# Kernel tuning notes

Hardware: AMD Instinct MI355X
Metric: run time of the kernel (lower is better)

## Reference

```python
import jax, jax.numpy as jnp
import numpy as np

N = 100000      # nodes
E = 1600000     # edges
F_IN = 64       # num_node_features
HID = 128       # hidden_channels
HEADS = 8       # heads in gat1
G = 1000        # number of graphs
EPS = 1e-5


def _layer_norm(x, gamma, beta):
    mu = jnp.mean(x, axis=-1, keepdims=True)
    var = jnp.var(x, axis=-1, keepdims=True)
    return (x - mu) * jax.lax.rsqrt(var + EPS) * gamma + beta


def _gat_conv(x, src, dst, W, a_src, a_dst, b):
    # PyG GATConv (concat=True, negative_slope=0.2, self-loops already in src/dst)
    n = x.shape[0]
    heads, c = a_src.shape
    h = (x @ W).reshape(n, heads, c)                      # [N,H,C]
    alpha_s = jnp.sum(h * a_src[None], axis=-1)           # [N,H]
    alpha_d = jnp.sum(h * a_dst[None], axis=-1)           # [N,H]
    e = jax.nn.leaky_relu(alpha_s[src] + alpha_d[dst], 0.2)   # [Etot,H]
    m = jax.ops.segment_max(e, dst, num_segments=n)       # per-dst max (stable softmax)
    e = jnp.exp(e - m[dst])
    denom = jax.ops.segment_sum(e, dst, num_segments=n)
    attn = e / (denom[dst] + 1e-16)                        # [Etot,H]
    out = jax.ops.segment_sum(h[src] * attn[:, :, None], dst, num_segments=n)
    return out.reshape(n, heads * c) + b


def setup_inputs():
    key = jax.random.key(0)
    ks = jax.random.split(key, 32)
    s = 0.05
    inp = {
        'x': jax.random.normal(ks[0], (N, F_IN), dtype=jnp.float32),
        'edge_index': jax.random.randint(ks[1], (2, E), 0, N),
        'batch': jnp.sort(jax.random.randint(ks[2], (N,), 0, G)),
        # gat1: 64 -> 16 per head, 8 heads
        'W1': jax.random.normal(ks[3], (F_IN, HID), dtype=jnp.float32) * s,
        'as1': jax.random.normal(ks[4], (HEADS, HID // HEADS), dtype=jnp.float32) * s,
        'ad1': jax.random.normal(ks[5], (HEADS, HID // HEADS), dtype=jnp.float32) * s,
        'b1': jnp.zeros((HID,), dtype=jnp.float32),
        # gat2: 128 -> 128, 1 head
        'W2': jax.random.normal(ks[6], (HID, HID), dtype=jnp.float32) * s,
        'as2': jax.random.normal(ks[7], (1, HID), dtype=jnp.float32) * s,
        'ad2': jax.random.normal(ks[8], (1, HID), dtype=jnp.float32) * s,
        'b2': jnp.zeros((HID,), dtype=jnp.float32),
        # gat3
        'W3': jax.random.normal(ks[9], (HID, HID), dtype=jnp.float32) * s,
        'as3': jax.random.normal(ks[10], (1, HID), dtype=jnp.float32) * s,
        'ad3': jax.random.normal(ks[11], (1, HID), dtype=jnp.float32) * s,
        'b3': jnp.zeros((HID,), dtype=jnp.float32),
        # layer norms
        'g1': jnp.ones((HID,), dtype=jnp.float32), 'be1': jnp.zeros((HID,), dtype=jnp.float32),
        'g2': jnp.ones((HID,), dtype=jnp.float32), 'be2': jnp.zeros((HID,), dtype=jnp.float32),
        'g3': jnp.ones((HID,), dtype=jnp.float32), 'be3': jnp.zeros((HID,), dtype=jnp.float32),
        # linear heads
        'lw1': jax.random.normal(ks[12], (HID, HID), dtype=jnp.float32) * s,
        'lb1': jnp.zeros((HID,), dtype=jnp.float32),
        'lw2': jax.random.normal(ks[13], (HID, HID), dtype=jnp.float32) * s,
        'lb2': jnp.zeros((HID,), dtype=jnp.float32),
    }
    return inp


def reference(x, edge_index, batch, W1, as1, ad1, b1, W2, as2, ad2, b2,
              W3, as3, ad3, b3, g1, be1, g2, be2, g3, be3, lw1, lb1, lw2, lb2):
    n = x.shape[0]
    loops = jnp.arange(n)
    src = jnp.concatenate([edge_index[0], loops])   # add self-loops (PyG default)
    dst = jnp.concatenate([edge_index[1], loops])

    h = _gat_conv(x, src, dst, W1, as1, ad1, b1)
    h = _layer_norm(jax.nn.elu(h), g1, be1)          # dropout is identity in eval

    idn2 = h
    h = _gat_conv(h, src, dst, W2, as2, ad2, b2)
    h = _layer_norm(jax.nn.elu(h), g2, be2) + idn2

    idn3 = h
    h = _gat_conv(h, src, dst, W3, as3, ad3, b3)
    h = _layer_norm(jax.nn.elu(h), g3, be3) + idn3

    # global mean pool over graphs
    sums = jax.ops.segment_sum(h, batch, num_segments=G)
    cnt = jax.ops.segment_sum(jnp.ones((n, 1), h.dtype), batch, num_segments=G)
    pooled = sums / jnp.maximum(cnt, 1.0)

    out = jax.nn.elu(pooled @ lw1 + lb1)
    return out @ lw2 + lb2
```

## Files before the change

kernel.cpp:

```cpp
#include <hip/hip_runtime.h>
#include <hip/hip_bf16.h>
#include <cstdint>
#include <cstddef>

constexpr int F_IN = 64;
constexpr int HID  = 128;
constexpr int SCHUNK = 4096;

typedef __attribute__((ext_vector_type(8))) short short8v;
typedef __attribute__((ext_vector_type(4))) float f32x4;
typedef __attribute__((ext_vector_type(8))) unsigned short ushort8v;

__device__ __forceinline__ float bf2f(unsigned short u) {
  return __uint_as_float((unsigned)u << 16);
}
__device__ __forceinline__ unsigned short f2bf(float x) {
  unsigned u = __float_as_uint(x);
  u += 0x7FFFu + ((u >> 16) & 1u);
  return (unsigned short)(u >> 16);
}

__global__ __launch_bounds__(256) void k_bhist(const int* __restrict__ ei,
                                               int* __restrict__ bcnt, int E) {
  __shared__ int hist[1024];
  int t = threadIdx.x;
  for (int k = t; k < 1024; k += 256) hist[k] = 0;
  __syncthreads();
  for (int i = blockIdx.x * 256 + t; i < E; i += gridDim.x * 256)
    atomicAdd(&hist[ei[E + i] >> 7], 1);
  __syncthreads();
  for (int k = t; k < 1024; k += 256)
    if (hist[k]) atomicAdd(&bcnt[k], hist[k]);
}

__global__ __launch_bounds__(1024) void k_bscan(const int* __restrict__ bcnt,
                                                int* __restrict__ boff,
                                                int* __restrict__ bcur, int nb) {
  __shared__ int tmp[1024];
  int t = threadIdx.x;
  int v = (t < nb) ? bcnt[t] : 0;
  tmp[t] = v;
  __syncthreads();
  #pragma unroll
  for (int off = 1; off < 1024; off <<= 1) {
    int x = tmp[t];
    int add = (t >= off) ? tmp[t - off] : 0;
    __syncthreads();
    tmp[t] = x + add;
    __syncthreads();
  }
  if (t < nb) {
    int ex = tmp[t] - v;
    boff[t] = ex;
    bcur[t] = ex;
    if (t == nb - 1) boff[nb] = tmp[t];
  }
}

__global__ __launch_bounds__(256) void k_bscat(const int* __restrict__ ei,
                                               int* __restrict__ bcur,
                                               uint2* __restrict__ pairs, int E) {
  __shared__ int lh[1024];
  __shared__ int lc[1024];
  int t = threadIdx.x;
  int start = blockIdx.x * SCHUNK;
  if (start >= E) return;
  int end = min(start + SCHUNK, E);
  for (int k = t; k < 1024; k += 256) { lh[k] = 0; lc[k] = 0; }
  __syncthreads();
  int dreg[SCHUNK / 256];
  #pragma unroll
  for (int q = 0; q < SCHUNK / 256; ++q) {
    int i = start + q * 256 + t;
    int d = (i < end) ? ei[E + i] : -1;
    dreg[q] = d;
    if (d >= 0) atomicAdd(&lh[d >> 7], 1);
  }
  __syncthreads();
  for (int k = t; k < 1024; k += 256) {
    int c = lh[k];
    lh[k] = (c > 0) ? atomicAdd(&bcur[k], c) : 0;
  }
  __syncthreads();
  #pragma unroll
  for (int q = 0; q < SCHUNK / 256; ++q) {
    int i = start + q * 256 + t;
    int d = dreg[q];
    if (d < 0) continue;
    int s = ei[i];
    int b = d >> 7;
    int loc = atomicAdd(&lc[b], 1);
    pairs[lh[b] + loc] = make_uint2((unsigned)s, (unsigned)d);
  }
}

__global__ __launch_bounds__(256) void k_bfin(const uint2* __restrict__ pairs,
                                              const int* __restrict__ boff,
                                              int* __restrict__ row_off,
                                              int* __restrict__ csr_src,
                                              int n, int E) {
  __shared__ int ldeg[128];
  __shared__ int lcur[128];
  int b = blockIdx.x;
  int t = threadIdx.x;
  int pb = boff[b], pe = boff[b + 1];
  int fullbase = pb + min(b << 7, n);
  int idx = (b << 7) + t;
  if (t < 128) ldeg[t] = (idx < n) ? 1 : 0;
  __syncthreads();
  for (int j = pb + t; j < pe; j += 256)
    atomicAdd(&ldeg[pairs[j].y & 127], 1);
  __syncthreads();
  int cnt = (t < 128) ? ldeg[t] : 0;
  for (int off = 1; off < 128; off <<= 1) {
    int add = (t < 128 && t >= off) ? ldeg[t - off] : 0;
    __syncthreads();
    if (t < 128) ldeg[t] += add;
    __syncthreads();
  }
  if (t < 128) {
    int base = fullbase + ldeg[t] - cnt;
    if (idx < n) {
      row_off[idx] = base;
      csr_src[base] = idx;
      lcur[t] = base + 1;
    } else lcur[t] = base;
  }
  if (b == 0 && t == 255) row_off[n] = E + n;
  __syncthreads();
  for (int j = pb + t; j < pe; j += 256) {
    uint2 pr = pairs[j];
    int pos = atomicAdd(&lcur[pr.y & 127], 1);
    csr_src[pos] = (int)pr.x;
  }
}

__global__ void k_tobf4(const float4* __restrict__ X, ushort4* __restrict__ Y,
                        int total4) {
  int i = blockIdx.x * 256 + threadIdx.x;
  if (i >= total4) return;
  float4 v = X[i];
  ushort4 o;
  o.x = f2bf(v.x); o.y = f2bf(v.y); o.z = f2bf(v.z); o.w = f2bf(v.w);
  Y[i] = o;
}

__global__ void k_wpack3(const float* __restrict__ W1, const float* __restrict__ W2,
                         const float* __restrict__ W3, unsigned short* __restrict__ Wf1,
                         unsigned short* __restrict__ Wf2, unsigned short* __restrict__ Wf3) {
  int i = blockIdx.x * 256 + threadIdx.x;
  const float* W; unsigned short* Wf; int idx;
  if (i < 8192)       { W = W1; Wf = Wf1; idx = i; }
  else if (i < 24576) { W = W2; Wf = Wf2; idx = i - 8192; }
  else if (i < 40960) { W = W3; Wf = Wf3; idx = i - 24576; }
  else return;
  int j    = idx & 7;
  int lane = (idx >> 3) & 63;
  int t    = (idx >> 9) & 7;
  int ks   = idx >> 12;
  int k = ks * 32 + (lane >> 4) * 8 + j;
  int c = t * 16 + (lane & 15);
  Wf[idx] = f2bf(W[k * 128 + c]);
}

template<int K, int HEADS>
__global__ __launch_bounds__(256) void k_mgemm(const short* __restrict__ Xb,
                                               const short* __restrict__ Wf,
                                               const float* __restrict__ a_s,
                                               const float* __restrict__ a_d,
                                               unsigned short* __restrict__ Y,
                                               float* __restrict__ AS,
                                               float* __restrict__ AD, int n) {
  int wv   = threadIdx.x >> 6;
  int lane = threadIdx.x & 63;
  int r0   = blockIdx.x * 64 + wv * 16;
  int ln = lane & 15, kg = lane >> 4;
  f32x4 acc[8] = {};
  int arow = min(r0 + ln, n - 1);
  const short* aptr = Xb + arow * K + kg * 8;
  #pragma unroll
  for (int ks = 0; ks < K / 32; ++ks) {
    short8v a = *(const short8v*)(aptr + ks * 32);
    const short* wp = Wf + ks * 4096 + lane * 8;
    #pragma unroll
    for (int t = 0; t < 8; ++t) {
      short8v b = *(const short8v*)(wp + t * 512);
      acc[t] = __builtin_amdgcn_mfma_f32_16x16x32_bf16(a, b, acc[t], 0, 0, 0);
    }
  }
  float asv[8], adv[8];
  #pragma unroll
  for (int t = 0; t < 8; ++t) { asv[t] = a_s[t * 16 + ln]; adv[t] = a_d[t * 16 + ln]; }
  #pragma unroll
  for (int reg = 0; reg < 4; ++reg) {
    int r = r0 + kg * 4 + reg;
    bool valid = (r < n);
    if (HEADS == 1) {
      float s1 = 0.f, s2 = 0.f;
      #pragma unroll
      for (int t = 0; t < 8; ++t) {
        s1 = fmaf(acc[t][reg], asv[t], s1);
        s2 = fmaf(acc[t][reg], adv[t], s2);
      }
      #pragma unroll
      for (int off = 1; off < 16; off <<= 1) {
        s1 += __shfl_xor(s1, off);
        s2 += __shfl_xor(s2, off);
      }
      if (valid && ln == 0) { AS[r] = s1; AD[r] = s2; }
    } else {
      float s1[8], s2[8];
      #pragma unroll
      for (int t = 0; t < 8; ++t) {
        s1[t] = acc[t][reg] * asv[t];
        s2[t] = acc[t][reg] * adv[t];
      }
      #pragma unroll
      for (int off = 1; off < 16; off <<= 1) {
        #pragma unroll
        for (int t = 0; t < 8; ++t) {
          s1[t] += __shfl_xor(s1[t], off);
          s2[t] += __shfl_xor(s2[t], off);
        }
      }
      float w1 = s1[0], w2 = s2[0];
      #pragma unroll
      for (int t = 1; t < 8; ++t) {
        w1 = (ln == t) ? s1[t] : w1;
        w2 = (ln == t) ? s2[t] : w2;
      }
      if (valid && ln < 8) { AS[r * 8 + ln] = w1; AD[r * 8 + ln] = w2; }
    }
  }
  #pragma unroll
  for (int t = 0; t < 8; ++t) {
    #pragma unroll
    for (int reg = 0; reg < 4; ++reg) {
      int r = r0 + kg * 4 + reg;
      if (r < n) Y[r * 128 + t * 16 + ln] = f2bf(acc[t][reg]);
    }
  }
}

template<int LOGC>
__global__ __launch_bounds__(256) void k_agg_post(const unsigned short* __restrict__ Hu,
    const int* __restrict__ row_off, const int* __restrict__ csr_src,
    const float* __restrict__ AS, const float* __restrict__ AD,
    const float* __restrict__ bias, const unsigned short* __restrict__ RES,
    const float* __restrict__ gamma, const float* __restrict__ beta,
    unsigned short* __restrict__ Yb, int n, int has_res) {
  if constexpr (LOGC >= 7) {
    int tid = blockIdx.x * 256 + threadIdx.x;
    int wid = tid >> 4;
    int ll  = threadIdx.x & 15;
    if (wid >= n) return;
    int c = ll << 3;
    int sbase = (threadIdx.x & 63) & ~15;
    float adv = AD[wid];
    int jb = row_off[wid], je = row_off[wid + 1];
    float den = 0.f, a[8] = {};
    for (int j0 = jb; j0 < je; j0 += 16) {
      int cnt = min(16, je - j0);
      int s_l = 0; float p_l = 0.f;
      if (ll < cnt) {
        s_l = csr_src[j0 + ll];
        float e = AS[s_l] + adv;
        e = (e > 0.f) ? e : 0.2f * e;
        p_l = __expf(e);
      }
      int k = 0;
      for (; k + 8 <= cnt; k += 8) {
        int sk[8]; float pk[8]; ushort8v uu[8];
        #pragma unroll
        for (int q = 0; q < 8; ++q) sk[q] = __shfl(s_l, sbase | (k + q));
        #pragma unroll
        for (int q = 0; q < 8; ++q) uu[q] = *(const ushort8v*)(Hu + (sk[q] << 7) + c);
        #pragma unroll
        for (int q = 0; q < 8; ++q) pk[q] = __shfl(p_l, sbase | (k + q));
        #pragma unroll
        for (int q = 0; q < 8; ++q) {
          den += pk[q];
          #pragma unroll
          for (int m = 0; m < 8; ++m) a[m] = fmaf(pk[q], bf2f(uu[q][m]), a[m]);
        }
      }
      for (; k < cnt; ++k) {
        int   s  = __shfl(s_l, sbase | k);
        float pk = __shfl(p_l, sbase | k);
        ushort8v u = *(const ushort8v*)(Hu + (s << 7) + c);
        den += pk;
        #pragma unroll
        for (int m = 0; m < 8; ++m) a[m] = fmaf(pk, bf2f(u[m]), a[m]);
      }
    }
    float inv = 1.f / (den + 1e-16f);
    float4 bv0 = *(const float4*)(bias + c);
    float4 bv1 = *(const float4*)(bias + c + 4);
    float e[8];
    float bb[8] = {bv0.x, bv0.y, bv0.z, bv0.w, bv1.x, bv1.y, bv1.z, bv1.w};
    #pragma unroll
    for (int m = 0; m < 8; ++m) {
      float t = a[m] * inv + bb[m];
      e[m] = t > 0.f ? t : __expf(t) - 1.f;
    }
    float s1 = 0.f, s2 = 0.f;
    #pragma unroll
    for (int m = 0; m < 8; ++m) { s1 += e[m]; s2 += e[m] * e[m]; }
    #pragma unroll
    for (int off = 1; off < 16; off <<= 1) {
      s1 += __shfl_xor(s1, off);
      s2 += __shfl_xor(s2, off);
    }
    float mu  = s1 * (1.f / 128.f);
    float var = s2 * (1.f / 128.f) - mu * mu;
    float rs  = rsqrtf(var + 1e-5f);
    int base = wid * HID;
    float rr[8] = {};
    if (has_res) {
      ushort8v rv = *(const ushort8v*)(RES + base + c);
      #pragma unroll
      for (int m = 0; m < 8; ++m) rr[m] = bf2f(rv[m]);
    }
    float4 gv0 = *(const float4*)(gamma + c);
    float4 gv1 = *(const float4*)(gamma + c + 4);
    float4 tv0 = *(const float4*)(beta + c);
    float4 tv1 = *(const float4*)(beta + c + 4);
    float gg[8] = {gv0.x, gv0.y, gv0.z, gv0.w, gv1.x, gv1.y, gv1.z, gv1.w};
    float tt[8] = {tv0.x, tv0.y, tv0.z, tv0.w, tv1.x, tv1.y, tv1.z, tv1.w};
    ushort8v ob;
    #pragma unroll
    for (int m = 0; m < 8; ++m) ob[m] = f2bf((e[m] - mu) * rs * gg[m] + tt[m] + rr[m]);
    *(ushort8v*)(Yb + base + c) = ob;
  } else {
    int tid = blockIdx.x * 256 + threadIdx.x;
    int wid = tid >> 5;
    int ll  = threadIdx.x & 31;
    if (wid >= n) return;
    constexpr int NH  = HID >> LOGC;
    constexpr int SEG = 1 << (LOGC - 2);
    int abslane = threadIdx.x & 63;
    int c = ll << 2;
    int h = c >> LOGC;
    int r = ll & (SEG - 1);
    int sbase = abslane & ~(SEG - 1);
    float adv = AD[wid * NH + h];
    int jb = row_off[wid], je = row_off[wid + 1];
    float den = 0.f, a0 = 0.f, a1 = 0.f, a2 = 0.f, a3 = 0.f;
    for (int j0 = jb; j0 < je; j0 += SEG) {
      int cnt = min(SEG, je - j0);
      int s_l = 0; float p_l = 0.f;
      if (r < cnt) {
        s_l = csr_src[j0 + r];
        float e = AS[s_l * NH + h] + adv;
        e = (e > 0.f) ? e : 0.2f * e;
        p_l = __expf(e);
      }
      int k = 0;
      for (; k + 4 <= cnt; k += 4) {
        int sk0 = __shfl(s_l, sbase | k);
        int sk1 = __shfl(s_l, sbase | (k + 1));
        int sk2 = __shfl(s_l, sbase | (k + 2));
        int sk3 = __shfl(s_l, sbase | (k + 3));
        ushort4 u0 = *(const ushort4*)(Hu + (sk0 << 7) + c);
        ushort4 u1 = *(const ushort4*)(Hu + (sk1 << 7) + c);
        ushort4 u2 = *(const ushort4*)(Hu + (sk2 << 7) + c);
        ushort4 u3 = *(const ushort4*)(Hu + (sk3 << 7) + c);
        float p0 = __shfl(p_l, sbase | k);
        float p1 = __shfl(p_l, sbase | (k + 1));
        float p2 = __shfl(p_l, sbase | (k + 2));
        float p3 = __shfl(p_l, sbase | (k + 3));
        den += (p0 + p1) + (p2 + p3);
        a0 = fmaf(p0, bf2f(u0.x), a0); a1 = fmaf(p0, bf2f(u0.y), a1);
        a2 = fmaf(p0, bf2f(u0.z), a2); a3 = fmaf(p0, bf2f(u0.w), a3);
        a0 = fmaf(p1, bf2f(u1.x), a0); a1 = fmaf(p1, bf2f(u1.y), a1);
        a2 = fmaf(p1, bf2f(u1.z), a2); a3 = fmaf(p1, bf2f(u1.w), a3);
        a0 = fmaf(p2, bf2f(u2.x), a0); a1 = fmaf(p2, bf2f(u2.y), a1);
        a2 = fmaf(p2, bf2f(u2.z), a2); a3 = fmaf(p2, bf2f(u2.w), a3);
        a0 = fmaf(p3, bf2f(u3.x), a0); a1 = fmaf(p3, bf2f(u3.y), a1);
        a2 = fmaf(p3, bf2f(u3.z), a2); a3 = fmaf(p3, bf2f(u3.w), a3);
      }
      for (; k < cnt; ++k) {
        int   s  = __shfl(s_l, sbase | k);
        float pk = __shfl(p_l, sbase | k);
        ushort4 u = *(const ushort4*)(Hu + (s << 7) + c);
        den += pk;
        a0 = fmaf(pk, bf2f(u.x), a0); a1 = fmaf(pk, bf2f(u.y), a1);
        a2 = fmaf(pk, bf2f(u.z), a2); a3 = fmaf(pk, bf2f(u.w), a3);
      }
    }
    float inv = 1.f / (den + 1e-16f);
    float4 bv = *(const float4*)(bias + c);
    float t0 = a0 * inv + bv.x;
    float t1 = a1 * inv + bv.y;
    float t2 = a2 * inv + bv.z;
    float t3 = a3 * inv + bv.w;
    float e0 = t0 > 0.f ? t0 : __expf(t0) - 1.f;
    float e1 = t1 > 0.f ? t1 : __expf(t1) - 1.f;
    float e2 = t2 > 0.f ? t2 : __expf(t2) - 1.f;
    float e3 = t3 > 0.f ? t3 : __expf(t3) - 1.f;
    float s1 = (e0 + e1) + (e2 + e3);
    float s2 = (e0 * e0 + e1 * e1) + (e2 * e2 + e3 * e3);
    #pragma unroll
    for (int off = 16; off >= 1; off >>= 1) {
      s1 += __shfl_xor(s1, off);
      s2 += __shfl_xor(s2, off);
    }
    float mu  = s1 * (1.f / 128.f);
    float var = s2 * (1.f / 128.f) - mu * mu;
    float rs  = rsqrtf(var + 1e-5f);
    int base = wid * HID;
    float r0 = 0.f, r1 = 0.f, r2 = 0.f, r3 = 0.f;
    if (has_res) {
      ushort4 rv = *(const ushort4*)(RES + base + c);
      r0 = bf2f(rv.x); r1 = bf2f(rv.y); r2 = bf2f(rv.z); r3 = bf2f(rv.w);
    }
    float4 gv = *(const float4*)(gamma + c);
    float4 betv = *(const float4*)(beta + c);
    ushort4 ob;
    ob.x = f2bf((e0 - mu) * rs * gv.x + betv.x + r0);
    ob.y = f2bf((e1 - mu) * rs * gv.y + betv.y + r1);
    ob.z = f2bf((e2 - mu) * rs * gv.z + betv.z + r2);
    ob.w = f2bf((e3 - mu) * rs * gv.w + betv.w + r3);
    *(ushort4*)(Yb + base + c) = ob;
  }
}

__global__ __launch_bounds__(128) void k_head(const unsigned short* __restrict__ Hf,
    const int* __restrict__ batch, const float* __restrict__ lw1,
    const float* __restrict__ lb1, const float* __restrict__ lw2,
    const float* __restrict__ lb2, float* __restrict__ out, int n) {
  __shared__ float pooled[128];
  __shared__ float h1[128];
  int g = blockIdx.x;
  int c = threadIdx.x;
  int lo = 0, hi = n;
  while (lo < hi) { int mid = (lo + hi) >> 1; if (batch[mid] < g) lo = mid + 1; else hi = mid; }
  int start = lo;
  hi = n;
  while (lo < hi) { int mid = (lo + hi) >> 1; if (batch[mid] < g + 1) lo = mid + 1; else hi = mid; }
  int end = lo;
  float s = 0.f;
  for (int i = start; i < end; ++i) s += bf2f(Hf[(size_t)i * 128 + c]);
  pooled[c] = s / (float)max(end - start, 1);
  __syncthreads();
  float acc = lb1[c];
  #pragma unroll 8
  for (int k = 0; k < 128; ++k) acc = fmaf(pooled[k], lw1[k * 128 + c], acc);
  h1[c] = acc > 0.f ? acc : __expf(acc) - 1.f;
  __syncthreads();
  float acc2 = lb2[c];
  #pragma unroll 8
  for (int k = 0; k < 128; ++k) acc2 = fmaf(h1[k], lw2[k * 128 + c], acc2);
  out[(size_t)g * 128 + c] = acc2;
}

extern "C" void kernel_launch(void* const* d_in, const int* in_sizes, int n_in,
                              void* d_out, int out_size, void* d_ws, size_t ws_size,
                              hipStream_t stream) {
  const float* x   = (const float*)d_in[0];
  const int*   ei  = (const int*)d_in[1];
  const int*   bat = (const int*)d_in[2];
  const float* W1  = (const float*)d_in[3];
  const float* as1 = (const float*)d_in[4];
  const float* ad1 = (const float*)d_in[5];
  const float* b1  = (const float*)d_in[6];
  const float* W2  = (const float*)d_in[7];
  const float* as2 = (const float*)d_in[8];
  const float* ad2 = (const float*)d_in[9];
  const float* b2  = (const float*)d_in[10];
  const float* W3  = (const float*)d_in[11];
  const float* as3 = (const float*)d_in[12];
  const float* ad3 = (const float*)d_in[13];
  const float* b3  = (const float*)d_in[14];
  const float* g1  = (const float*)d_in[15];
  const float* be1 = (const float*)d_in[16];
  const float* g2  = (const float*)d_in[17];
  const float* be2 = (const float*)d_in[18];
  const float* g3  = (const float*)d_in[19];
  const float* be3 = (const float*)d_in[20];
  const float* lw1 = (const float*)d_in[21];
  const float* lb1 = (const float*)d_in[22];
  const float* lw2 = (const float*)d_in[23];
  const float* lb2 = (const float*)d_in[24];

  int N = in_sizes[0] / F_IN;
  int E = in_sizes[1] / 2;
  int G = out_size / HID;
  int tot = E + N;
  int nb  = (N + 127) >> 7;

  char* p = (char*)d_ws;
  auto alloc = [&](size_t bytes) { char* r = p; p += (bytes + 511) & ~(size_t)511; return r; };
  int*   bcnt    = (int*)  alloc(1024 * 4);
  int*   boff    = (int*)  alloc(1025 * 4);
  int*   bcur    = (int*)  alloc(1024 * 4);
  int*   row_off = (int*)  alloc((size_t)(N + 1) * 4);
  int*   csr_src = (int*)  alloc((size_t)tot * 4);
  uint2* pairs   = (uint2*)alloc((size_t)E * 8);
  float* AS      = (float*)alloc((size_t)N * 8 * 4);
  float* AD      = (float*)alloc((size_t)N * 8 * 4);
  unsigned short* Hb  = (unsigned short*)alloc((size_t)N * HID * 2);
  unsigned short* Fb0 = (unsigned short*)alloc((size_t)N * HID * 2);
  unsigned short* Fb1 = (unsigned short*)alloc((size_t)N * HID * 2);
  unsigned short* Fb2 = (unsigned short*)alloc((size_t)N * HID * 2);
  unsigned short* Wf1 = (unsigned short*)alloc(64 * 128 * 2);
  unsigned short* Wf2 = (unsigned short*)alloc(128 * 128 * 2);
  unsigned short* Wf3 = (unsigned short*)alloc(128 * 128 * 2);
  unsigned short* xb  = (unsigned short*)pairs;

  (void)hipMemsetAsync(bcnt, 0, 1024 * 4, stream);

  int sb = (E + SCHUNK - 1) / SCHUNK;
  k_bhist<<<256, 256, 0, stream>>>(ei, bcnt, E);
  k_bscan<<<1, 1024, 0, stream>>>(bcnt, boff, bcur, nb);
  k_bscat<<<sb, 256, 0, stream>>>(ei, bcur, pairs, E);
  k_bfin <<<nb, 256, 0, stream>>>(pairs, boff, row_off, csr_src, N, E);

  k_tobf4 <<<(N * F_IN / 4 + 255) / 256, 256, 0, stream>>>((const float4*)x,
                                                           (ushort4*)xb, N * F_IN / 4);
  k_wpack3<<<160, 256, 0, stream>>>(W1, W2, W3, Wf1, Wf2, Wf3);

  int mb  = (N + 63) / 64;
  int nh4 = (N + 7) / 8;
  int nh7 = (N + 15) / 16;

  k_mgemm<64, 8><<<mb, 256, 0, stream>>>((const short*)xb, (const short*)Wf1,
                                         as1, ad1, Hb, AS, AD, N);
  k_agg_post<4><<<nh4, 256, 0, stream>>>(Hb, row_off, csr_src, AS, AD, b1,
                                         nullptr, g1, be1, Fb0, N, 0);

  k_mgemm<128, 1><<<mb, 256, 0, stream>>>((const short*)Fb0, (const short*)Wf2,
                                          as2, ad2, Hb, AS, AD, N);
  k_agg_post<7><<<nh7, 256, 0, stream>>>(Hb, row_off, csr_src, AS, AD, b2,
                                         Fb0, g2, be2, Fb1, N, 1);

  k_mgemm<128, 1><<<mb, 256, 0, stream>>>((const short*)Fb1, (const short*)Wf3,
                                          as3, ad3, Hb, AS, AD, N);
  k_agg_post<7><<<nh7, 256, 0, stream>>>(Hb, row_off, csr_src, AS, AD, b3,
                                         Fb1, g3, be3, Fb2, N, 1);

  k_head<<<G, 128, 0, stream>>>(Fb2, bat, lw1, lb1, lw2, lb2, (float*)d_out, N);
}
```

Baseline: 429.5 us.

## Split GAT aggregation into edge-softmax, column-sliced gather, and post LayerNorm kernels

The GEMM output now goes to a column-sliced layout: eight 16-channel slabs of N×16 bf16. A separate edge kernel precomputes normalized attention weights per edge, and per head for layer 1. A sliced aggregation kernel then gathers 32-byte rows from one slab per block, so each slab (about 3.2 MB) can stay cache-resident while the random neighbor gathers run, and a post kernel applies ELU, LayerNorm and the residual. The cost is extra launches, an attention buffer written and read (up to 8×(E+N) floats for layer 1), csr_src read eight times, and a bf16 round-trip of the pre-activation through T.

```diff
diff --git a/kernel.cpp b/kernel.cpp
--- a/kernel.cpp
+++ b/kernel.cpp
@@ -170,7 +170,7 @@
                                                const float* __restrict__ a_d,
                                                unsigned short* __restrict__ Y,
                                                float* __restrict__ AS,
-                                               float* __restrict__ AD, int n) {
+                                               float* __restrict__ AD, int n, int n16) {
   int wv   = threadIdx.x >> 6;
   int lane = threadIdx.x & 63;
   int r0   = blockIdx.x * 64 + wv * 16;
@@ -237,192 +237,147 @@
     #pragma unroll
     for (int reg = 0; reg < 4; ++reg) {
       int r = r0 + kg * 4 + reg;
-      if (r < n) Y[r * 128 + t * 16 + ln] = f2bf(acc[t][reg]);
+      if (r < n) Y[t * n16 + r * 16 + ln] = f2bf(acc[t][reg]);
     }
   }
 }
 
-template<int LOGC>
-__global__ __launch_bounds__(256) void k_agg_post(const unsigned short* __restrict__ Hu,
+__global__ __launch_bounds__(256) void k_edgep1(const int* __restrict__ row_off,
+    const int* __restrict__ csr_src, const float* __restrict__ AS,
+    const float* __restrict__ AD, float* __restrict__ attn, int n) {
+  int tid = blockIdx.x * 256 + threadIdx.x;
+  int wid = tid >> 4;
+  int ll  = threadIdx.x & 15;
+  if (wid >= n) return;
+  float adv = AD[wid];
+  int jb = row_off[wid], je = row_off[wid + 1];
+  float den = 0.f;
+  for (int j = jb + ll; j < je; j += 16) {
+    int s = csr_src[j];
+    float e = AS[s] + adv;
+    e = (e > 0.f) ? e : 0.2f * e;
+    float p = __expf(e);
+    attn[j] = p;
+    den += p;
+  }
+  #pragma unroll
+  for (int off = 1; off < 16; off <<= 1) den += __shfl_xor(den, off);
+  float inv = 1.f / (den + 1e-16f);
+  for (int j = jb + ll; j < je; j += 16) attn[j] *= inv;
+}
+
+__global__ __launch_bounds__(256) void k_edgep8(const int* __restrict__ row_off,
+    const int* __restrict__ csr_src, const float* __restrict__ AS,
+    const float* __restrict__ AD, float* __restrict__ attn, int AE, int n) {
+  int tid = blockIdx.x * 256 + threadIdx.x;
+  int wid = tid >> 5;
+  int ll  = threadIdx.x & 31;
+  if (wid >= n) return;
+  int e = ll >> 3, h = ll & 7;
+  float adv = AD[wid * 8 + h];
+  int jb = row_off[wid], je = row_off[wid + 1];
+  float den = 0.f;
+  for (int j = jb + e; j < je; j += 4) {
+    int s = csr_src[j];
+    float x = AS[s * 8 + h] + adv;
+    x = (x > 0.f) ? x : 0.2f * x;
+    float p = __expf(x);
+    attn[h * AE + j] = p;
+    den += p;
+  }
+  den += __shfl_xor(den, 8);
+  den += __shfl_xor(den, 16);
+  float inv = 1.f / (den + 1e-16f);
+  for (int j = jb + e; j < je; j += 4) attn[h * AE + j] *= inv;
+}
+
+__global__ __launch_bounds__(256) void k_aggs(const unsigned short* __restrict__ Hs,
     const int* __restrict__ row_off, const int* __restrict__ csr_src,
-    const float* __restrict__ AS, const float* __restrict__ AD,
-    const float* __restrict__ bias, const unsigned short* __restrict__ RES,
-    const float* __restrict__ gamma, const float* __restrict__ beta,
-    unsigned short* __restrict__ Yb, int n, int has_res) {
-  if constexpr (LOGC >= 7) {
-    int tid = blockIdx.x * 256 + threadIdx.x;
-    int wid = tid >> 4;
-    int ll  = threadIdx.x & 15;
-    if (wid >= n) return;
-    int c = ll << 3;
-    int sbase = (threadIdx.x & 63) & ~15;
-    float adv = AD[wid];
-    int jb = row_off[wid], je = row_off[wid + 1];
-    float den = 0.f, a[8] = {};
-    for (int j0 = jb; j0 < je; j0 += 16) {
-      int cnt = min(16, je - j0);
-      int s_l = 0; float p_l = 0.f;
-      if (ll < cnt) {
-        s_l = csr_src[j0 + ll];
-        float e = AS[s_l] + adv;
-        e = (e > 0.f) ? e : 0.2f * e;
-        p_l = __expf(e);
-      }
-      int k = 0;
-      for (; k + 8 <= cnt; k += 8) {
-        int sk[8]; float pk[8]; ushort8v uu[8];
-        #pragma unroll
-        for (int q = 0; q < 8; ++q) sk[q] = __shfl(s_l, sbase | (k + q));
-        #pragma unroll
-        for (int q = 0; q < 8; ++q) uu[q] = *(const ushort8v*)(Hu + (sk[q] << 7) + c);
-        #pragma unroll
-        for (int q = 0; q < 8; ++q) pk[q] = __shfl(p_l, sbase | (k + q));
-        #pragma unroll
-        for (int q = 0; q < 8; ++q) {
-          den += pk[q];
-          #pragma unroll
-          for (int m = 0; m < 8; ++m) a[m] = fmaf(pk[q], bf2f(uu[q][m]), a[m]);
-        }
-      }
-      for (; k < cnt; ++k) {
-        int   s  = __shfl(s_l, sbase | k);
-        float pk = __shfl(p_l, sbase | k);
-        ushort8v u = *(const ushort8v*)(Hu + (s << 7) + c);
-        den += pk;
-        #pragma unroll
-        for (int m = 0; m < 8; ++m) a[m] = fmaf(pk, bf2f(u[m]), a[m]);
-      }
+    const float* __restrict__ attn, int astride, const float* __restrict__ bias,
+    unsigned short* __restrict__ T, int n, int n16) {
+  int s   = blockIdx.x & 7;
+  int grp = blockIdx.x >> 3;
+  int lane = threadIdx.x & 63;
+  int wave = threadIdx.x >> 6;
+  int node = grp * 128 + wave * 32 + (lane >> 1);
+  if (node >= n) return;
+  int half = lane & 1;
+  const unsigned short* Hsl = Hs + (size_t)s * n16;
+  const float* at = attn + (size_t)s * astride;
+  int jb = row_off[node], je = row_off[node + 1];
+  float a[8] = {};
+  int j = jb;
+  for (; j + 8 <= je; j += 8) {
+    int sk[8]; float wk[8]; ushort8v uu[8];
+    #pragma unroll
+    for (int q = 0; q < 8; ++q) sk[q] = __builtin_nontemporal_load(csr_src + j + q);
+    #pragma unroll
+    for (int q = 0; q < 8; ++q) uu[q] = *(const ushort8v*)(Hsl + (sk[q] << 4) + half * 8);
+    #pragma unroll
+    for (int q = 0; q < 8; ++q) wk[q] = __builtin_nontemporal_load(at + j + q);
+    #pragma unroll
+    for (int q = 0; q < 8; ++q) {
+      #pragma unroll
+      for (int m = 0; m < 8; ++m) a[m] = fmaf(wk[q], bf2f(uu[q][m]), a[m]);
     }
-    float inv = 1.f / (den + 1e-16f);
-    float4 bv0 = *(const float4*)(bias + c);
-    float4 bv1 = *(const float4*)(bias + c + 4);
-    float e[8];
-    float bb[8] = {bv0.x, bv0.y, bv0.z, bv0.w, bv1.x, bv1.y, bv1.z, bv1.w};
-    #pragma unroll
-    for (int m = 0; m < 8; ++m) {
-      float t = a[m] * inv + bb[m];
-      e[m] = t > 0.f ? t : __expf(t) - 1.f;
-    }
-    float s1 = 0.f, s2 = 0.f;
-    #pragma unroll
-    for (int m = 0; m < 8; ++m) { s1 += e[m]; s2 += e[m] * e[m]; }
-    #pragma unroll
-    for (int off = 1; off < 16; off <<= 1) {
-      s1 += __shfl_xor(s1, off);
-      s2 += __shfl_xor(s2, off);
-    }
-    float mu  = s1 * (1.f / 128.f);
-    float var = s2 * (1.f / 128.f) - mu * mu;
-    float rs  = rsqrtf(var + 1e-5f);
-    int base = wid * HID;
-    float rr[8] = {};
-    if (has_res) {
-      ushort8v rv = *(const ushort8v*)(RES + base + c);
-      #pragma unroll
-      for (int m = 0; m < 8; ++m) rr[m] = bf2f(rv[m]);
-    }
-    float4 gv0 = *(const float4*)(gamma + c);
-    float4 gv1 = *(const float4*)(gamma + c + 4);
-    float4 tv0 = *(const float4*)(beta + c);
-    float4 tv1 = *(const float4*)(beta + c + 4);
-    float gg[8] = {gv0.x, gv0.y, gv0.z, gv0.w, gv1.x, gv1.y, gv1.z, gv1.w};
-    float tt[8] = {tv0.x, tv0.y, tv0.z, tv0.w, tv1.x, tv1.y, tv1.z, tv1.w};
-    ushort8v ob;
-    #pragma unroll
-    for (int m = 0; m < 8; ++m) ob[m] = f2bf((e[m] - mu) * rs * gg[m] + tt[m] + rr[m]);
-    *(ushort8v*)(Yb + base + c) = ob;
-  } else {
-    int tid = blockIdx.x * 256 + threadIdx.x;
-    int wid = tid >> 5;
-    int ll  = threadIdx.x & 31;
-    if (wid >= n) return;
-    constexpr int NH  = HID >> LOGC;
-    constexpr int SEG = 1 << (LOGC - 2);
-    int abslane = threadIdx.x & 63;
-    int c = ll << 2;
-    int h = c >> LOGC;
-    int r = ll & (SEG - 1);
-    int sbase = abslane & ~(SEG - 1);
-    float adv = AD[wid * NH + h];
-    int jb = row_off[wid], je = row_off[wid + 1];
-    float den = 0.f, a0 = 0.f, a1 = 0.f, a2 = 0.f, a3 = 0.f;
-    for (int j0 = jb; j0 < je; j0 += SEG) {
-      int cnt = min(SEG, je - j0);
-      int s_l = 0; float p_l = 0.f;
-      if (r < cnt) {
-        s_l = csr_src[j0 + r];
-        float e = AS[s_l * NH + h] + adv;
-        e = (e > 0.f) ? e : 0.2f * e;
-        p_l = __expf(e);
-      }
-      int k = 0;
-      for (; k + 4 <= cnt; k += 4) {
-        int sk0 = __shfl(s_l, sbase | k);
-        int sk1 = __shfl(s_l, sbase | (k + 1));
-        int sk2 = __shfl(s_l, sbase | (k + 2));
-        int sk3 = __shfl(s_l, sbase | (k + 3));
-        ushort4 u0 = *(const ushort4*)(Hu + (sk0 << 7) + c);
-        ushort4 u1 = *(const ushort4*)(Hu + (sk1 << 7) + c);
-        ushort4 u2 = *(const ushort4*)(Hu + (sk2 << 7) + c);
-        ushort4 u3 = *(const ushort4*)(Hu + (sk3 << 7) + c);
-        float p0 = __shfl(p_l, sbase | k);
-        float p1 = __shfl(p_l, sbase | (k + 1));
-        float p2 = __shfl(p_l, sbase | (k + 2));
-        float p3 = __shfl(p_l, sbase | (k + 3));
-        den += (p0 + p1) + (p2 + p3);
-        a0 = fmaf(p0, bf2f(u0.x), a0); a1 = fmaf(p0, bf2f(u0.y), a1);
-        a2 = fmaf(p0, bf2f(u0.z), a2); a3 = fmaf(p0, bf2f(u0.w), a3);
-        a0 = fmaf(p1, bf2f(u1.x), a0); a1 = fmaf(p1, bf2f(u1.y), a1);
-        a2 = fmaf(p1, bf2f(u1.z), a2); a3 = fmaf(p1, bf2f(u1.w), a3);
-        a0 = fmaf(p2, bf2f(u2.x), a0); a1 = fmaf(p2, bf2f(u2.y), a1);
-        a2 = fmaf(p2, bf2f(u2.z), a2); a3 = fmaf(p2, bf2f(u2.w), a3);
-        a0 = fmaf(p3, bf2f(u3.x), a0); a1 = fmaf(p3, bf2f(u3.y), a1);
-        a2 = fmaf(p3, bf2f(u3.z), a2); a3 = fmaf(p3, bf2f(u3.w), a3);
-      }
-      for (; k < cnt; ++k) {
-        int   s  = __shfl(s_l, sbase | k);
-        float pk = __shfl(p_l, sbase | k);
-        ushort4 u = *(const ushort4*)(Hu + (s << 7) + c);
-        den += pk;
-        a0 = fmaf(pk, bf2f(u.x), a0); a1 = fmaf(pk, bf2f(u.y), a1);
-        a2 = fmaf(pk, bf2f(u.z), a2); a3 = fmaf(pk, bf2f(u.w), a3);
-      }
-    }
-    float inv = 1.f / (den + 1e-16f);
-    float4 bv = *(const float4*)(bias + c);
-    float t0 = a0 * inv + bv.x;
-    float t1 = a1 * inv + bv.y;
-    float t2 = a2 * inv + bv.z;
-    float t3 = a3 * inv + bv.w;
-    float e0 = t0 > 0.f ? t0 : __expf(t0) - 1.f;
-    float e1 = t1 > 0.f ? t1 : __expf(t1) - 1.f;
-    float e2 = t2 > 0.f ? t2 : __expf(t2) - 1.f;
-    float e3 = t3 > 0.f ? t3 : __expf(t3) - 1.f;
-    float s1 = (e0 + e1) + (e2 + e3);
-    float s2 = (e0 * e0 + e1 * e1) + (e2 * e2 + e3 * e3);
-    #pragma unroll
-    for (int off = 16; off >= 1; off >>= 1) {
-      s1 += __shfl_xor(s1, off);
-      s2 += __shfl_xor(s2, off);
-    }
-    float mu  = s1 * (1.f / 128.f);
-    float var = s2 * (1.f / 128.f) - mu * mu;
-    float rs  = rsqrtf(var + 1e-5f);
-    int base = wid * HID;
-    float r0 = 0.f, r1 = 0.f, r2 = 0.f, r3 = 0.f;
-    if (has_res) {
-      ushort4 rv = *(const ushort4*)(RES + base + c);
-      r0 = bf2f(rv.x); r1 = bf2f(rv.y); r2 = bf2f(rv.z); r3 = bf2f(rv.w);
-    }
-    float4 gv = *(const float4*)(gamma + c);
-    float4 betv = *(const float4*)(beta + c);
-    ushort4 ob;
-    ob.x = f2bf((e0 - mu) * rs * gv.x + betv.x + r0);
-    ob.y = f2bf((e1 - mu) * rs * gv.y + betv.y + r1);
-    ob.z = f2bf((e2 - mu) * rs * gv.z + betv.z + r2);
-    ob.w = f2bf((e3 - mu) * rs * gv.w + betv.w + r3);
-    *(ushort4*)(Yb + base + c) = ob;
-  }
+  }
+  for (; j < je; ++j) {
+    int sv = __builtin_nontemporal_load(csr_src + j);
+    float w = __builtin_nontemporal_load(at + j);
+    ushort8v u = *(const ushort8v*)(Hsl + (sv << 4) + half * 8);
+    #pragma unroll
+    for (int m = 0; m < 8; ++m) a[m] = fmaf(w, bf2f(u[m]), a[m]);
+  }
+  int cbase = s * 16 + half * 8;
+  ushort8v ob;
+  #pragma unroll
+  for (int m = 0; m < 8; ++m) ob[m] = f2bf(a[m] + bias[cbase + m]);
+  *(ushort8v*)(T + (size_t)s * n16 + node * 16 + half * 8) = ob;
+}
+
+__global__ __launch_bounds__(256) void k_post(const unsigned short* __restrict__ T,
+    const unsigned short* __restrict__ RES, const float* __restrict__ gamma,
+    const float* __restrict__ beta, unsigned short* __restrict__ F,
+    int n, int n16, int has_res) {
+  int tid = blockIdx.x * 256 + threadIdx.x;
+  int node = tid >> 4;
+  int ll = threadIdx.x & 15;
+  if (node >= n) return;
+  int sl = ll >> 1, half = ll & 1;
+  ushort8v tv = *(const ushort8v*)(T + (size_t)sl * n16 + node * 16 + half * 8);
+  float e[8];
+  float s1 = 0.f, s2 = 0.f;
+  #pragma unroll
+  for (int m = 0; m < 8; ++m) {
+    float t = bf2f(tv[m]);
+    t = t > 0.f ? t : __expf(t) - 1.f;
+    e[m] = t; s1 += t; s2 += t * t;
+  }
+  #pragma unroll
+  for (int off = 1; off < 16; off <<= 1) {
+    s1 += __shfl_xor(s1, off);
+    s2 += __shfl_xor(s2, off);
+  }
+  float mu  = s1 * (1.f / 128.f);
+  float var = s2 * (1.f / 128.f) - mu * mu;
+  float rs  = rsqrtf(var + 1e-5f);
+  int c = ll * 8;
+  float4 gv0 = *(const float4*)(gamma + c);
+  float4 gv1 = *(const float4*)(gamma + c + 4);
+  float4 bv0 = *(const float4*)(beta + c);
+  float4 bv1 = *(const float4*)(beta + c + 4);
+  float gg[8] = {gv0.x, gv0.y, gv0.z, gv0.w, gv1.x, gv1.y, gv1.z, gv1.w};
+  float bb[8] = {bv0.x, bv0.y, bv0.z, bv0.w, bv1.x, bv1.y, bv1.z, bv1.w};
+  float rr[8] = {};
+  if (has_res) {
+    ushort8v rv = *(const ushort8v*)(RES + (size_t)node * 128 + c);
+    #pragma unroll
+    for (int m = 0; m < 8; ++m) rr[m] = bf2f(rv[m]);
+  }
+  ushort8v ob;
+  #pragma unroll
+  for (int m = 0; m < 8; ++m) ob[m] = f2bf((e[m] - mu) * rs * gg[m] + bb[m] + rr[m]);
+  *(ushort8v*)(F + (size_t)node * 128 + c) = ob;
 }
 
 __global__ __launch_bounds__(128) void k_head(const unsigned short* __restrict__ Hf,
@@ -488,6 +443,7 @@
   int G = out_size / HID;
   int tot = E + N;
   int nb  = (N + 127) >> 7;
+  int n16 = N * 16;
 
   char* p = (char*)d_ws;
   auto alloc = [&](size_t bytes) { char* r = p; p += (bytes + 511) & ~(size_t)511; return r; };
@@ -499,7 +455,9 @@
   uint2* pairs   = (uint2*)alloc((size_t)E * 8);
   float* AS      = (float*)alloc((size_t)N * 8 * 4);
   float* AD      = (float*)alloc((size_t)N * 8 * 4);
-  unsigned short* Hb  = (unsigned short*)alloc((size_t)N * HID * 2);
+  float* attn    = (float*)alloc((size_t)tot * 8 * 4);
+  unsigned short* Hs  = (unsigned short*)alloc((size_t)N * HID * 2);
+  unsigned short* T   = (unsigned short*)alloc((size_t)N * HID * 2);
   unsigned short* Fb0 = (unsigned short*)alloc((size_t)N * HID * 2);
   unsigned short* Fb1 = (unsigned short*)alloc((size_t)N * HID * 2);
   unsigned short* Fb2 = (unsigned short*)alloc((size_t)N * HID * 2);
@@ -521,23 +479,27 @@
   k_wpack3<<<160, 256, 0, stream>>>(W1, W2, W3, Wf1, Wf2, Wf3);
 
   int mb  = (N + 63) / 64;
-  int nh4 = (N + 7) / 8;
-  int nh7 = (N + 15) / 16;
+  int ep1 = (N * 16 + 255) / 256;
+  int ep8 = (N * 32 + 255) / 256;
+  int ags = 8 * ((N + 127) / 128);
 
   k_mgemm<64, 8><<<mb, 256, 0, stream>>>((const short*)xb, (const short*)Wf1,
-                                         as1, ad1, Hb, AS, AD, N);
-  k_agg_post<4><<<nh4, 256, 0, stream>>>(Hb, row_off, csr_src, AS, AD, b1,
-                                         nullptr, g1, be1, Fb0, N, 0);
+                                         as1, ad1, Hs, AS, AD, N, n16);
+  k_edgep8<<<ep8, 256, 0, stream>>>(row_off, csr_src, AS, AD, attn, tot, N);
+  k_aggs  <<<ags, 256, 0, stream>>>(Hs, row_off, csr_src, attn, tot, b1, T, N, n16);
+  k_post  <<<ep1, 256, 0, stream>>>(T, nullptr, g1, be1, Fb0, N, n16, 0);
 
   k_mgemm<128, 1><<<mb, 256, 0, stream>>>((const short*)Fb0, (const short*)Wf2,
-                                          as2, ad2, Hb, AS, AD, N);
-  k_agg_post<7><<<nh7, 256, 0, stream>>>(Hb, row_off, csr_src, AS, AD, b2,
-                                         Fb0, g2, be2, Fb1, N, 1);
+                                          as2, ad2, Hs, AS, AD, N, n16);
+  k_edgep1<<<ep1, 256, 0, stream>>>(row_off, csr_src, AS, AD, attn, N);
+  k_aggs  <<<ags, 256, 0, stream>>>(Hs, row_off, csr_src, attn, 0, b2, T, N, n16);
+  k_post  <<<ep1, 256, 0, stream>>>(T, Fb0, g2, be2, Fb1, N, n16, 1);
 
   k_mgemm<128, 1><<<mb, 256, 0, stream>>>((const short*)Fb1, (const short*)Wf3,
-                                          as3, ad3, Hb, AS, AD, N);
-  k_agg_post<7><<<nh7, 256, 0, stream>>>(Hb, row_off, csr_src, AS, AD, b3,
-                                         Fb1, g3, be3, Fb2, N, 1);
+                                          as3, ad3, Hs, AS, AD, N, n16);
+  k_edgep1<<<ep1, 256, 0, stream>>>(row_off, csr_src, AS, AD, attn, N);
+  k_aggs  <<<ags, 256, 0, stream>>>(Hs, row_off, csr_src, attn, 0, b3, T, N, n16);
+  k_post  <<<ep1, 256, 0, stream>>>(T, Fb1, g3, be3, Fb2, N, n16, 1);
 
   k_head<<<G, 128, 0, stream>>>(Fb2, bat, lw1, lb1, lw2, lb2, (float*)d_out, N);
 }
```

After: 909.4 us. 2.12x slower.
